# Performance work log

Measured on AMD Instinct MI355X. Metric: run time of the kernel, lower is better.

The kernel has to match this reference:

```python
import jax, jax.numpy as jnp
import numpy as np

L, N, C, F, H = 6, 16384, 8, 128, 128


def setup_inputs() -> dict:
    key = jax.random.key(0)
    ks = jax.random.split(key, 8)
    node_features = jax.random.normal(ks[0], (L, N, F), dtype=jnp.float32)
    # child indices point into the hidden states of the level below
    child_idx = jax.random.randint(ks[1], (L, N, C), 0, N)
    # random child masks; bottom level (processed first) has no children (leaves)
    child_mask = jax.random.randint(ks[2], (L, N, C), 0, 2).astype(bool)
    child_mask = child_mask.at[L - 1].set(False)
    A_c = jax.random.uniform(ks[3], (L, N, C, C), dtype=jnp.float32)
    s = 1.0 / np.sqrt(H)
    W_g = jax.random.normal(ks[4], (H, H), dtype=jnp.float32) * s
    W_ih = jax.random.normal(ks[5], (F, H), dtype=jnp.float32) * s
    W_hh = jax.random.normal(ks[6], (H, H), dtype=jnp.float32) * s
    b_ih = jnp.zeros((H,), dtype=jnp.float32)
    b_hh = jnp.zeros((H,), dtype=jnp.float32)
    return {
        "node_features": node_features, "child_idx": child_idx,
        "child_mask": child_mask, "A_c": A_c,
        "W_g": W_g, "W_ih": W_ih, "W_hh": W_hh,
        "b_ih": b_ih, "b_hh": b_hh,
    }


def reference(node_features, child_idx, child_mask, A_c, W_g, W_ih, W_hh, b_ih, b_hh):
    # Level-wise (bottom-up) batched form of deepFirstConvolution:
    #   gather child hiddens -> edge graph conv -> masked maxpool readout -> RNN update
    neg = jnp.finfo(node_features.dtype).min

    def step(h_below, level):  # h_below: [N, H]
        x, cidx, cmask, a = level
        ch = h_below[cidx] * cmask[..., None]              # [N, C, H] gather + zero-pad
        g = jax.nn.relu(jnp.einsum('ncd,ndh->nch', a, ch) @ W_g)  # edge graph conv
        pooled = jnp.where(cmask[..., None], g, neg).max(axis=1)  # maxpool readout [N, H]
        has_child = cmask.any(axis=1, keepdims=True)
        pooled = jnp.where(has_child, pooled, 0.0)         # leaves get zero init hiddens
        h_new = jnp.tanh(x @ W_ih + b_ih + pooled @ W_hh + b_hh)  # RNN update
        return h_new, None

    # process from deepest level (index L-1) up to the root level (index 0)
    levels = (node_features[::-1], child_idx[::-1], child_mask[::-1], A_c[::-1])
    h0 = jnp.zeros((node_features.shape[1], W_hh.shape[0]), dtype=node_features.dtype)
    root_hiddens, _ = jax.lax.scan(step, h0, levels)
    return root_hiddens  # [N, H]
```

## Files before the change

kernel.cpp:

```cpp
#include <hip/hip_runtime.h>
#include <cfloat>

#define LL 6
#define NN 16384
#define CC 8
#define FF 128
#define HH 128
#define BN 16

typedef __bf16 bf16x8 __attribute__((ext_vector_type(8)));
typedef __attribute__((ext_vector_type(4))) float f32x4;

static __device__ inline unsigned short f2bfbits(float f) {
    return __builtin_bit_cast(unsigned short, (__bf16)f);
}
static __device__ inline float bfbits2f(unsigned short b) {
    return (float)__builtin_bit_cast(__bf16, b);
}

__global__ void detect_mask_kernel(const unsigned int* __restrict__ raw,
                                   int* __restrict__ flag) {
    __shared__ int any;
    if (threadIdx.x == 0) any = 0;
    __syncthreads();
    const unsigned int a = raw[threadIdx.x * 2 + 0];
    const unsigned int b = raw[threadIdx.x * 2 + 1];
    if (((a | b) & 0xFFFFFF00u) != 0) atomicOr(&any, 1);
    __syncthreads();
    if (threadIdx.x == 0) *flag = any ? 0 : 1;
}

__global__ void mask_bits_kernel(const unsigned char* __restrict__ raw,
                                 const int* __restrict__ flag,
                                 unsigned char* __restrict__ mbits) {
    const int n = blockIdx.x * blockDim.x + threadIdx.x;
    if (n >= LL * NN) return;
    const int f = *flag;
    unsigned char b;
    if (f) {
        const uint4 v0 = *(const uint4*)(raw + (size_t)n * 32);
        const uint4 v1 = *(const uint4*)(raw + (size_t)n * 32 + 16);
        b = (v0.x ? 1 : 0) | (v0.y ? 2 : 0) | (v0.z ? 4 : 0) | (v0.w ? 8 : 0)
          | (v1.x ? 16 : 0) | (v1.y ? 32 : 0) | (v1.z ? 64 : 0) | (v1.w ? 128 : 0);
    } else {
        const unsigned a = *(const unsigned*)(raw + (size_t)n * 8);
        const unsigned c = *(const unsigned*)(raw + (size_t)n * 8 + 4);
        b = ((a & 0xFFu) ? 1 : 0) | ((a & 0xFF00u) ? 2 : 0)
          | ((a & 0xFF0000u) ? 4 : 0) | ((a >> 24) ? 8 : 0)
          | ((c & 0xFFu) ? 16 : 0) | ((c & 0xFF00u) ? 32 : 0)
          | ((c & 0xFF0000u) ? 64 : 0) | ((c >> 24) ? 128 : 0);
    }
    mbits[n] = b;
}

__global__ void pack_weights_kernel(const float* __restrict__ Wg,
                                    const float* __restrict__ Wih,
                                    const float* __restrict__ Whh,
                                    const float* __restrict__ bih,
                                    const float* __restrict__ bhh,
                                    unsigned short* __restrict__ WgHi,
                                    unsigned short* __restrict__ WgLo,
                                    unsigned short* __restrict__ WdHi,
                                    unsigned short* __restrict__ WdLo,
                                    float* __restrict__ bias) {
    const int t = blockIdx.x * 256 + threadIdx.x;
    if (t < 2048) {
        const int l = t & 63;
        const int nt = t >> 8;
        const int kt = (t >> 6) & 3;
        const int n = nt * 16 + (l & 15);
        const int kb = kt * 32 + (l >> 4) * 8;
        #pragma unroll
        for (int i = 0; i < 8; ++i) {
            const float v = Wg[(kb + i) * HH + n];
            const unsigned short hb = f2bfbits(v);
            WgHi[t * 8 + i] = hb;
            WgLo[t * 8 + i] = f2bfbits(v - bfbits2f(hb));
        }
    } else if (t < 6144) {
        const int u = t - 2048;
        const int l = u & 63;
        const int nt = u >> 9;
        const int kt = (u >> 6) & 7;
        const int n = nt * 16 + (l & 15);
        const int kb = (kt & 3) * 32 + (l >> 4) * 8;
        const float* W = (kt < 4) ? Wih : Whh;
        #pragma unroll
        for (int i = 0; i < 8; ++i) {
            const float v = W[(kb + i) * HH + n];
            const unsigned short hb = f2bfbits(v);
            WdHi[u * 8 + i] = hb;
            WdLo[u * 8 + i] = f2bfbits(v - bfbits2f(hb));
        }
    } else if (t < 6272) {
        const int n = t - 6144;
        bias[n] = bih[n] + bhh[n];
    }
}

#define SWZ(row, byte) ((unsigned)(((row) * 256 + (byte)) ^ (((row) & 7) << 4)))

__global__ __launch_bounds__(256) void level_kernel(
    const float* __restrict__ x_l,
    const int* __restrict__ cidx_l,
    const unsigned char* __restrict__ mbits_l,
    const float* __restrict__ Hp_in,
    const float* __restrict__ a_l,
    const unsigned short* __restrict__ WgHi,
    const unsigned short* __restrict__ WgLo,
    const unsigned short* __restrict__ WdHi,
    const unsigned short* __restrict__ WdLo,
    const float* __restrict__ bias,
    float* __restrict__ h_out,
    float* __restrict__ Hp_out)
{
    __shared__ __align__(16) unsigned char pH[BN * 256];
    __shared__ __align__(16) unsigned char pL[BN * 256];
    __shared__ __align__(16) unsigned char hH[BN * 256];
    __shared__ __align__(16) unsigned char hL[BN * 256];
    __shared__ float a_lds[BN][CC][CC];
    __shared__ int   cidx_lds[BN][CC];
    __shared__ __align__(16) unsigned char maskbyte[BN];

    const int tid = threadIdx.x;
    const int lane = tid & 63;
    const int w = tid >> 6;
    const int lrow = lane & 15, lgrp = lane >> 4;
    const long nbase = (long)blockIdx.x * BN;

    ((float4*)a_lds)[tid] = ((const float4*)(a_l + nbase * CC * CC))[tid];
    if (tid < 32)
        ((uint4*)cidx_lds)[tid] = ((const uint4*)(cidx_l + nbase * CC))[tid];
    if (tid < BN) maskbyte[tid] = mbits_l[nbase + tid];

    float4 xr[8];
    #pragma unroll
    for (int kt = 0; kt < 4; ++kt) {
        const float* src = &x_l[(nbase + lrow) * FF + kt * 32 + lgrp * 8];
        xr[kt * 2 + 0] = *(const float4*)src;
        xr[kt * 2 + 1] = *(const float4*)(src + 4);
    }
    __syncthreads();

    const uint4 mball = *(const uint4*)maskbyte;
    const int any = (mball.x | mball.y | mball.z | mball.w) != 0;

    if (any) {
        for (int nl = 0; nl < 4; ++nl) {
            const int node = w * 4 + nl;
            const int mb = maskbyte[node];
            float m0 = 0.f, m1 = 0.f;
            if (mb) {
                float c0[CC], c1[CC];
                #pragma unroll
                for (int c = 0; c < CC; ++c) { c0[c] = 0.f; c1[c] = 0.f; }
                #pragma unroll
                for (int c = 0; c < CC; ++c) {
                    if (mb & (1 << c)) {
                        const float2 v = *(const float2*)&Hp_in[(size_t)cidx_lds[node][c] * HH + 2 * lane];
                        c0[c] = v.x; c1[c] = v.y;
                    }
                }
                float mm0 = -FLT_MAX, mm1 = -FLT_MAX;
                #pragma unroll
                for (int c = 0; c < CC; ++c) {
                    if (mb & (1 << c)) {
                        float s0 = 0.f, s1 = 0.f;
                        #pragma unroll
                        for (int d = 0; d < CC; ++d) {
                            const float av = a_lds[node][c][d];
                            s0 += av * c0[d]; s1 += av * c1[d];
                        }
                        mm0 = fmaxf(mm0, fmaxf(s0, 0.f));
                        mm1 = fmaxf(mm1, fmaxf(s1, 0.f));
                    }
                }
                m0 = mm0; m1 = mm1;
            }
            const unsigned short h0 = f2bfbits(m0);
            const unsigned short h1 = f2bfbits(m1);
            const unsigned short l0 = f2bfbits(m0 - bfbits2f(h0));
            const unsigned short l1 = f2bfbits(m1 - bfbits2f(h1));
            const unsigned off = SWZ(node, lane * 4);
            *(unsigned*)&pH[off] = (unsigned)h0 | ((unsigned)h1 << 16);
            *(unsigned*)&pL[off] = (unsigned)l0 | ((unsigned)l1 << 16);
        }
        __syncthreads();
    }

    bf16x8 ah[8], al[8];
    #pragma unroll
    for (int kt = 0; kt < 4; ++kt) {
        const float4 v0 = xr[kt * 2 + 0];
        const float4 v1 = xr[kt * 2 + 1];
        const float vv[8] = {v0.x, v0.y, v0.z, v0.w, v1.x, v1.y, v1.z, v1.w};
        bf16x8 hfr, lfr;
        #pragma unroll
        for (int i = 0; i < 8; ++i) {
            const __bf16 hb = (__bf16)vv[i];
            hfr[i] = hb;
            lfr[i] = (__bf16)(vv[i] - (float)hb);
        }
        ah[kt] = hfr; al[kt] = lfr;
    }
    if (any) {
        #pragma unroll
        for (int kt = 4; kt < 8; ++kt) {
            const unsigned off = SWZ(lrow, (kt - 4) * 64 + lgrp * 16);
            ah[kt] = *(const bf16x8*)&pH[off];
            al[kt] = *(const bf16x8*)&pL[off];
        }
    }
    float hv[2][4];
    #pragma unroll
    for (int nn = 0; nn < 2; ++nn) {
        const int nt = w * 2 + nn;
        f32x4 acc = {0.f, 0.f, 0.f, 0.f};
        #pragma unroll
        for (int kt = 0; kt < 4; ++kt) {
            const bf16x8 bh = *(const bf16x8*)&WdHi[((nt * 8 + kt) * 64 + lane) * 8];
            const bf16x8 bl = *(const bf16x8*)&WdLo[((nt * 8 + kt) * 64 + lane) * 8];
            acc = __builtin_amdgcn_mfma_f32_16x16x32_bf16(ah[kt], bh, acc, 0, 0, 0);
            acc = __builtin_amdgcn_mfma_f32_16x16x32_bf16(ah[kt], bl, acc, 0, 0, 0);
            acc = __builtin_amdgcn_mfma_f32_16x16x32_bf16(al[kt], bh, acc, 0, 0, 0);
        }
        if (any) {
            #pragma unroll
            for (int kt = 4; kt < 8; ++kt) {
                const bf16x8 bh = *(const bf16x8*)&WdHi[((nt * 8 + kt) * 64 + lane) * 8];
                const bf16x8 bl = *(const bf16x8*)&WdLo[((nt * 8 + kt) * 64 + lane) * 8];
                acc = __builtin_amdgcn_mfma_f32_16x16x32_bf16(ah[kt], bh, acc, 0, 0, 0);
                acc = __builtin_amdgcn_mfma_f32_16x16x32_bf16(ah[kt], bl, acc, 0, 0, 0);
                acc = __builtin_amdgcn_mfma_f32_16x16x32_bf16(al[kt], bh, acc, 0, 0, 0);
            }
        }
        const float b = bias[nt * 16 + lrow];
        #pragma unroll
        for (int r = 0; r < 4; ++r) {
            const float h = tanhf(acc[r] + b);
            hv[nn][r] = h;
            h_out[(nbase + lgrp * 4 + r) * HH + nt * 16 + lrow] = h;
        }
    }

    if (Hp_out != nullptr) {
        #pragma unroll
        for (int nn = 0; nn < 2; ++nn) {
            #pragma unroll
            for (int r = 0; r < 4; ++r) {
                const int row = lgrp * 4 + r;
                const int col = (w * 2 + nn) * 16 + lrow;
                const unsigned short hb = f2bfbits(hv[nn][r]);
                const unsigned short lb = f2bfbits(hv[nn][r] - bfbits2f(hb));
                const unsigned off = SWZ(row, col * 2);
                *(unsigned short*)&hH[off] = hb;
                *(unsigned short*)&hL[off] = lb;
            }
        }
        __syncthreads();
        bf16x8 aHh[4], aLh[4];
        #pragma unroll
        for (int kt = 0; kt < 4; ++kt) {
            const unsigned off = SWZ(lrow, kt * 64 + lgrp * 16);
            aHh[kt] = *(const bf16x8*)&hH[off];
            aLh[kt] = *(const bf16x8*)&hL[off];
        }
        #pragma unroll
        for (int nn = 0; nn < 2; ++nn) {
            const int nt = w * 2 + nn;
            f32x4 acc = {0.f, 0.f, 0.f, 0.f};
            #pragma unroll
            for (int kt = 0; kt < 4; ++kt) {
                const bf16x8 bh = *(const bf16x8*)&WgHi[((nt * 4 + kt) * 64 + lane) * 8];
                const bf16x8 bl = *(const bf16x8*)&WgLo[((nt * 4 + kt) * 64 + lane) * 8];
                acc = __builtin_amdgcn_mfma_f32_16x16x32_bf16(aHh[kt], bh, acc, 0, 0, 0);
                acc = __builtin_amdgcn_mfma_f32_16x16x32_bf16(aHh[kt], bl, acc, 0, 0, 0);
                acc = __builtin_amdgcn_mfma_f32_16x16x32_bf16(aLh[kt], bh, acc, 0, 0, 0);
            }
            #pragma unroll
            for (int r = 0; r < 4; ++r)
                Hp_out[(nbase + lgrp * 4 + r) * HH + nt * 16 + lrow] = acc[r];
        }
    }
}

extern "C" void kernel_launch(void* const* d_in, const int* in_sizes, int n_in,
                              void* d_out, int out_size, void* d_ws, size_t ws_size,
                              hipStream_t stream) {
    const float* node_features = (const float*)d_in[0];
    const int*   child_idx     = (const int*)d_in[1];
    const unsigned char* child_mask_raw = (const unsigned char*)d_in[2];
    const float* A_c  = (const float*)d_in[3];
    const float* Wg   = (const float*)d_in[4];
    const float* Wih  = (const float*)d_in[5];
    const float* Whh  = (const float*)d_in[6];
    const float* bih  = (const float*)d_in[7];
    const float* bhh  = (const float*)d_in[8];
    float* out = (float*)d_out;

    char* ws = (char*)d_ws;
    int* flag = (int*)ws;
    unsigned char* mbits = (unsigned char*)(ws + 256);
    unsigned short* WgHi = (unsigned short*)(ws + (1 << 20));
    unsigned short* WgLo = (unsigned short*)(ws + (1 << 20) + (32 << 10));
    unsigned short* WdHi = (unsigned short*)(ws + (1 << 20) + (64 << 10));
    unsigned short* WdLo = (unsigned short*)(ws + (1 << 20) + (128 << 10));
    float* bias          = (float*)(ws + (1 << 20) + (192 << 10));
    float* hbuf          = (float*)(ws + (1 << 20) + (256 << 10));
    float* HpA           = (float*)(ws + (1 << 20) + (256 << 10) + (8 << 20));
    float* HpB           = (float*)(ws + (1 << 20) + (256 << 10) + (16 << 20));

    detect_mask_kernel<<<1, 256, 0, stream>>>((const unsigned int*)child_mask_raw, flag);
    mask_bits_kernel<<<(LL * NN + 255) / 256, 256, 0, stream>>>(
        child_mask_raw, flag, mbits);
    pack_weights_kernel<<<25, 256, 0, stream>>>(Wg, Wih, Whh, bih, bhh,
                                                WgHi, WgLo, WdHi, WdLo, bias);

    for (int s = 0; s < LL; ++s) {
        const int l = LL - 1 - s;
        float* ho = (s & 1) ? out : hbuf;
        float* hp_in  = (s & 1) ? HpB : HpA;
        float* hp_out = (s & 1) ? HpA : HpB;
        level_kernel<<<NN / BN, 256, 0, stream>>>(
            node_features + (size_t)l * NN * FF,
            child_idx     + (size_t)l * NN * CC,
            mbits         + (size_t)l * NN,
            hp_in,
            A_c           + (size_t)l * NN * CC * CC,
            WgHi, WgLo, WdHi, WdLo, bias,
            ho,
            (s == LL - 1) ? nullptr : hp_out);
    }
}
```

Baseline: 154.2 us.

## Merge prologue kernels, skip intermediate hidden writes, reuse LDS, fast tanh

Folds the mask-detect, mask-pack and weight-pack kernels into one prologue launch, which cuts two launches. Only the final level now writes hidden states to global memory, so intermediate levels stop storing h. The hidden-state LDS buffers are dropped in favour of the pooled buffers, at the cost of an extra barrier. The x loads move next to their use, and tanhf is replaced by an exp-based fast tanh that may lose some accuracy.

New measurement: 139.2 us. -9.8%, faster.

```diff
diff --git a/kernel.cpp b/kernel.cpp
--- a/kernel.cpp
+++ b/kernel.cpp
@@ -17,68 +17,69 @@
 static __device__ inline float bfbits2f(unsigned short b) {
     return (float)__builtin_bit_cast(__bf16, b);
 }
-
-__global__ void detect_mask_kernel(const unsigned int* __restrict__ raw,
-                                   int* __restrict__ flag) {
-    __shared__ int any;
-    if (threadIdx.x == 0) any = 0;
-    __syncthreads();
-    const unsigned int a = raw[threadIdx.x * 2 + 0];
-    const unsigned int b = raw[threadIdx.x * 2 + 1];
-    if (((a | b) & 0xFFFFFF00u) != 0) atomicOr(&any, 1);
-    __syncthreads();
-    if (threadIdx.x == 0) *flag = any ? 0 : 1;
-}
-
-__global__ void mask_bits_kernel(const unsigned char* __restrict__ raw,
-                                 const int* __restrict__ flag,
-                                 unsigned char* __restrict__ mbits) {
-    const int n = blockIdx.x * blockDim.x + threadIdx.x;
-    if (n >= LL * NN) return;
-    const int f = *flag;
-    unsigned char b;
-    if (f) {
+static __device__ inline float fast_tanh(float x) {
+    const float e = __expf(2.0f * x);
+    return 1.0f - __fdividef(2.0f, e + 1.0f);
+}
+
+#define SWZ(row, byte) ((unsigned)(((row) * 256 + (byte)) ^ (((row) & 7) << 4)))
+
+__device__ inline unsigned char make_maskbyte(const unsigned char* raw,
+                                              int n, int f_i32) {
+    if (f_i32) {
         const uint4 v0 = *(const uint4*)(raw + (size_t)n * 32);
         const uint4 v1 = *(const uint4*)(raw + (size_t)n * 32 + 16);
-        b = (v0.x ? 1 : 0) | (v0.y ? 2 : 0) | (v0.z ? 4 : 0) | (v0.w ? 8 : 0)
-          | (v1.x ? 16 : 0) | (v1.y ? 32 : 0) | (v1.z ? 64 : 0) | (v1.w ? 128 : 0);
+        return (v0.x ? 1 : 0) | (v0.y ? 2 : 0) | (v0.z ? 4 : 0) | (v0.w ? 8 : 0)
+             | (v1.x ? 16 : 0) | (v1.y ? 32 : 0) | (v1.z ? 64 : 0) | (v1.w ? 128 : 0);
     } else {
         const unsigned a = *(const unsigned*)(raw + (size_t)n * 8);
         const unsigned c = *(const unsigned*)(raw + (size_t)n * 8 + 4);
-        b = ((a & 0xFFu) ? 1 : 0) | ((a & 0xFF00u) ? 2 : 0)
-          | ((a & 0xFF0000u) ? 4 : 0) | ((a >> 24) ? 8 : 0)
-          | ((c & 0xFFu) ? 16 : 0) | ((c & 0xFF00u) ? 32 : 0)
-          | ((c & 0xFF0000u) ? 64 : 0) | ((c >> 24) ? 128 : 0);
-    }
-    mbits[n] = b;
-}
-
-__global__ void pack_weights_kernel(const float* __restrict__ Wg,
-                                    const float* __restrict__ Wih,
-                                    const float* __restrict__ Whh,
-                                    const float* __restrict__ bih,
-                                    const float* __restrict__ bhh,
-                                    unsigned short* __restrict__ WgHi,
-                                    unsigned short* __restrict__ WgLo,
-                                    unsigned short* __restrict__ WdHi,
-                                    unsigned short* __restrict__ WdLo,
-                                    float* __restrict__ bias) {
-    const int t = blockIdx.x * 256 + threadIdx.x;
-    if (t < 2048) {
-        const int l = t & 63;
-        const int nt = t >> 8;
-        const int kt = (t >> 6) & 3;
+        return ((a & 0xFFu) ? 1 : 0) | ((a & 0xFF00u) ? 2 : 0)
+             | ((a & 0xFF0000u) ? 4 : 0) | ((a >> 24) ? 8 : 0)
+             | ((c & 0xFFu) ? 16 : 0) | ((c & 0xFF00u) ? 32 : 0)
+             | ((c & 0xFF0000u) ? 64 : 0) | ((c >> 24) ? 128 : 0);
+    }
+}
+
+__global__ __launch_bounds__(256) void prologue_kernel(
+    const unsigned char* __restrict__ mask_raw,
+    const float* __restrict__ Wg, const float* __restrict__ Wih,
+    const float* __restrict__ Whh,
+    const float* __restrict__ bih, const float* __restrict__ bhh,
+    unsigned char* __restrict__ mbits,
+    unsigned short* __restrict__ WgHi, unsigned short* __restrict__ WgLo,
+    unsigned short* __restrict__ WdHi, unsigned short* __restrict__ WdLo,
+    float* __restrict__ bias) {
+    __shared__ int s_any;
+    const int tid = threadIdx.x;
+    if (tid == 0) s_any = 0;
+    __syncthreads();
+    {
+        const unsigned a = ((const unsigned*)mask_raw)[tid * 2 + 0];
+        const unsigned b = ((const unsigned*)mask_raw)[tid * 2 + 1];
+        if (((a | b) & 0xFFFFFF00u) != 0) atomicOr(&s_any, 1);
+    }
+    __syncthreads();
+    const int f_i32 = s_any ? 0 : 1;
+
+    const int g = blockIdx.x * 256 + tid;
+    if (g < LL * NN) mbits[g] = make_maskbyte(mask_raw, g, f_i32);
+
+    if (g < 2048) {
+        const int l = g & 63;
+        const int nt = g >> 8;
+        const int kt = (g >> 6) & 3;
         const int n = nt * 16 + (l & 15);
         const int kb = kt * 32 + (l >> 4) * 8;
         #pragma unroll
         for (int i = 0; i < 8; ++i) {
             const float v = Wg[(kb + i) * HH + n];
             const unsigned short hb = f2bfbits(v);
-            WgHi[t * 8 + i] = hb;
-            WgLo[t * 8 + i] = f2bfbits(v - bfbits2f(hb));
-        }
-    } else if (t < 6144) {
-        const int u = t - 2048;
+            WgHi[g * 8 + i] = hb;
+            WgLo[g * 8 + i] = f2bfbits(v - bfbits2f(hb));
+        }
+    } else if (g < 6144) {
+        const int u = g - 2048;
         const int l = u & 63;
         const int nt = u >> 9;
         const int kt = (u >> 6) & 7;
@@ -92,32 +93,24 @@
             WdHi[u * 8 + i] = hb;
             WdLo[u * 8 + i] = f2bfbits(v - bfbits2f(hb));
         }
-    } else if (t < 6272) {
-        const int n = t - 6144;
+    } else if (g < 6272) {
+        const int n = g - 6144;
         bias[n] = bih[n] + bhh[n];
     }
 }
 
-#define SWZ(row, byte) ((unsigned)(((row) * 256 + (byte)) ^ (((row) & 7) << 4)))
-
 __global__ __launch_bounds__(256) void level_kernel(
-    const float* __restrict__ x_l,
-    const int* __restrict__ cidx_l,
+    const float* __restrict__ x_l, const int* __restrict__ cidx_l,
     const unsigned char* __restrict__ mbits_l,
-    const float* __restrict__ Hp_in,
-    const float* __restrict__ a_l,
-    const unsigned short* __restrict__ WgHi,
-    const unsigned short* __restrict__ WgLo,
-    const unsigned short* __restrict__ WdHi,
-    const unsigned short* __restrict__ WdLo,
+    const float* __restrict__ Hp_in, const float* __restrict__ a_l,
+    const unsigned short* __restrict__ WgHi, const unsigned short* __restrict__ WgLo,
+    const unsigned short* __restrict__ WdHi, const unsigned short* __restrict__ WdLo,
     const float* __restrict__ bias,
     float* __restrict__ h_out,
     float* __restrict__ Hp_out)
 {
     __shared__ __align__(16) unsigned char pH[BN * 256];
     __shared__ __align__(16) unsigned char pL[BN * 256];
-    __shared__ __align__(16) unsigned char hH[BN * 256];
-    __shared__ __align__(16) unsigned char hL[BN * 256];
     __shared__ float a_lds[BN][CC][CC];
     __shared__ int   cidx_lds[BN][CC];
     __shared__ __align__(16) unsigned char maskbyte[BN];
@@ -132,14 +125,6 @@
     if (tid < 32)
         ((uint4*)cidx_lds)[tid] = ((const uint4*)(cidx_l + nbase * CC))[tid];
     if (tid < BN) maskbyte[tid] = mbits_l[nbase + tid];
-
-    float4 xr[8];
-    #pragma unroll
-    for (int kt = 0; kt < 4; ++kt) {
-        const float* src = &x_l[(nbase + lrow) * FF + kt * 32 + lgrp * 8];
-        xr[kt * 2 + 0] = *(const float4*)src;
-        xr[kt * 2 + 1] = *(const float4*)(src + 4);
-    }
     __syncthreads();
 
     const uint4 mball = *(const uint4*)maskbyte;
@@ -191,8 +176,9 @@
     bf16x8 ah[8], al[8];
     #pragma unroll
     for (int kt = 0; kt < 4; ++kt) {
-        const float4 v0 = xr[kt * 2 + 0];
-        const float4 v1 = xr[kt * 2 + 1];
+        const float* src = &x_l[(nbase + lrow) * FF + kt * 32 + lgrp * 8];
+        const float4 v0 = *(const float4*)src;
+        const float4 v1 = *(const float4*)(src + 4);
         const float vv[8] = {v0.x, v0.y, v0.z, v0.w, v1.x, v1.y, v1.z, v1.w};
         bf16x8 hfr, lfr;
         #pragma unroll
@@ -236,14 +222,21 @@
         }
         const float b = bias[nt * 16 + lrow];
         #pragma unroll
-        for (int r = 0; r < 4; ++r) {
-            const float h = tanhf(acc[r] + b);
-            hv[nn][r] = h;
-            h_out[(nbase + lgrp * 4 + r) * HH + nt * 16 + lrow] = h;
-        }
-    }
-
+        for (int r = 0; r < 4; ++r)
+            hv[nn][r] = fast_tanh(acc[r] + b);
+    }
+
+    if (h_out != nullptr) {
+        #pragma unroll
+        for (int nn = 0; nn < 2; ++nn) {
+            const int nt = w * 2 + nn;
+            #pragma unroll
+            for (int r = 0; r < 4; ++r)
+                h_out[(nbase + lgrp * 4 + r) * HH + nt * 16 + lrow] = hv[nn][r];
+        }
+    }
     if (Hp_out != nullptr) {
+        __syncthreads();
         #pragma unroll
         for (int nn = 0; nn < 2; ++nn) {
             #pragma unroll
@@ -253,8 +246,8 @@
                 const unsigned short hb = f2bfbits(hv[nn][r]);
                 const unsigned short lb = f2bfbits(hv[nn][r] - bfbits2f(hb));
                 const unsigned off = SWZ(row, col * 2);
-                *(unsigned short*)&hH[off] = hb;
-                *(unsigned short*)&hL[off] = lb;
+                *(unsigned short*)&pH[off] = hb;
+                *(unsigned short*)&pL[off] = lb;
             }
         }
         __syncthreads();
@@ -262,8 +255,8 @@
         #pragma unroll
         for (int kt = 0; kt < 4; ++kt) {
             const unsigned off = SWZ(lrow, kt * 64 + lgrp * 16);
-            aHh[kt] = *(const bf16x8*)&hH[off];
-            aLh[kt] = *(const bf16x8*)&hL[off];
+            aHh[kt] = *(const bf16x8*)&pH[off];
+            aLh[kt] = *(const bf16x8*)&pL[off];
         }
         #pragma unroll
         for (int nn = 0; nn < 2; ++nn) {
@@ -287,48 +280,42 @@
 extern "C" void kernel_launch(void* const* d_in, const int* in_sizes, int n_in,
                               void* d_out, int out_size, void* d_ws, size_t ws_size,
                               hipStream_t stream) {
-    const float* node_features = (const float*)d_in[0];
-    const int*   child_idx     = (const int*)d_in[1];
-    const unsigned char* child_mask_raw = (const unsigned char*)d_in[2];
+    const float* nf   = (const float*)d_in[0];
+    const int*   cidx = (const int*)d_in[1];
+    const unsigned char* mraw = (const unsigned char*)d_in[2];
     const float* A_c  = (const float*)d_in[3];
     const float* Wg   = (const float*)d_in[4];
     const float* Wih  = (const float*)d_in[5];
     const float* Whh  = (const float*)d_in[6];
     const float* bih  = (const float*)d_in[7];
     const float* bhh  = (const float*)d_in[8];
-    float* out = (float*)d_out;
+    float* outp = (float*)d_out;
 
     char* ws = (char*)d_ws;
-    int* flag = (int*)ws;
-    unsigned char* mbits = (unsigned char*)(ws + 256);
-    unsigned short* WgHi = (unsigned short*)(ws + (1 << 20));
-    unsigned short* WgLo = (unsigned short*)(ws + (1 << 20) + (32 << 10));
-    unsigned short* WdHi = (unsigned short*)(ws + (1 << 20) + (64 << 10));
-    unsigned short* WdLo = (unsigned short*)(ws + (1 << 20) + (128 << 10));
-    float* bias          = (float*)(ws + (1 << 20) + (192 << 10));
-    float* hbuf          = (float*)(ws + (1 << 20) + (256 << 10));
-    float* HpA           = (float*)(ws + (1 << 20) + (256 << 10) + (8 << 20));
-    float* HpB           = (float*)(ws + (1 << 20) + (256 << 10) + (16 << 20));
-
-    detect_mask_kernel<<<1, 256, 0, stream>>>((const unsigned int*)child_mask_raw, flag);
-    mask_bits_kernel<<<(LL * NN + 255) / 256, 256, 0, stream>>>(
-        child_mask_raw, flag, mbits);
-    pack_weights_kernel<<<25, 256, 0, stream>>>(Wg, Wih, Whh, bih, bhh,
-                                                WgHi, WgLo, WdHi, WdLo, bias);
+    unsigned char* mbits = (unsigned char*)ws;
+    unsigned short* WgHi = (unsigned short*)(ws + (128 << 10));
+    unsigned short* WgLo = (unsigned short*)(ws + (160 << 10));
+    unsigned short* WdHi = (unsigned short*)(ws + (192 << 10));
+    unsigned short* WdLo = (unsigned short*)(ws + (256 << 10));
+    float* bias          = (float*)(ws + (320 << 10));
+    float* HpA           = (float*)(ws + (1 << 20));
+    float* HpB           = (float*)(ws + (1 << 20) + (8 << 20));
+
+    prologue_kernel<<<(LL * NN) / 256, 256, 0, stream>>>(
+        mraw, Wg, Wih, Whh, bih, bhh, mbits, WgHi, WgLo, WdHi, WdLo, bias);
 
     for (int s = 0; s < LL; ++s) {
         const int l = LL - 1 - s;
-        float* ho = (s & 1) ? out : hbuf;
         float* hp_in  = (s & 1) ? HpB : HpA;
         float* hp_out = (s & 1) ? HpA : HpB;
         level_kernel<<<NN / BN, 256, 0, stream>>>(
-            node_features + (size_t)l * NN * FF,
-            child_idx     + (size_t)l * NN * CC,
-            mbits         + (size_t)l * NN,
+            nf   + (size_t)l * NN * FF,
+            cidx + (size_t)l * NN * CC,
+            mbits + (size_t)l * NN,
             hp_in,
-            A_c           + (size_t)l * NN * CC * CC,
+            A_c  + (size_t)l * NN * CC * CC,
             WgHi, WgLo, WdHi, WdLo, bias,
-            ho,
+            (s == LL - 1) ? outp : nullptr,
             (s == LL - 1) ? nullptr : hp_out);
     }
 }
```
